# Kernel optimization log

Hardware: AMD Instinct MI355X
Metric: run time of the kernel (lower is better)

The kernel has to match this reference:

```python
import jax, jax.numpy as jnp
import numpy as np

B, T, C = 2, 2048, 1024
N_HEAD = 16
HEAD_DIM = C // N_HEAD


def setup_inputs() -> dict:
    key = jax.random.key(0)
    k1, k2, k3 = jax.random.split(key, 3)
    x = jax.random.normal(k1, (B, T, C), dtype=jnp.float32)
    w_qkv = jax.random.normal(k2, (C, 3 * C), dtype=jnp.float32) * (C ** -0.5)
    w_proj = jax.random.normal(k3, (C, C), dtype=jnp.float32) * (C ** -0.5)
    b_proj = jnp.zeros((C,), dtype=jnp.float32)
    return {"x": x, "w_qkv": w_qkv, "w_proj": w_proj, "b_proj": b_proj}


def reference(x, w_qkv, w_proj, b_proj):
    Bx, Tx, Cx = x.shape
    # qkv projection: [B,T,3C] -> split into q,k,v each [B,H,T,D]
    qkv = x @ w_qkv  # [B,T,3C]
    qkv = qkv.reshape(Bx, Tx, 3, N_HEAD, HEAD_DIM)
    q = qkv[:, :, 0].transpose(0, 2, 1, 3)  # [B,H,T,D]
    k = qkv[:, :, 1].transpose(0, 2, 1, 3)
    v = qkv[:, :, 2].transpose(0, 2, 1, 3)
    scale = 1.0 / np.sqrt(HEAD_DIM).astype(np.float32)
    att = jnp.einsum('bhtd,bhsd->bhts', q, k) * scale  # [B,H,T,T]
    causal = jnp.tril(jnp.ones((Tx, Tx), dtype=bool))
    att = jnp.where(causal[None, None], att, -jnp.inf)
    att = jax.nn.softmax(att, axis=-1)
    # dropout p=0.0 -> identity (eval-mode math)
    y = jnp.einsum('bhts,bhsd->bhtd', att, v)  # [B,H,T,D]
    y = y.transpose(0, 2, 1, 3).reshape(Bx, Tx, Cx)
    return y @ w_proj + b_proj
```

## Files before the change

### kernel.cpp

```cpp
#include <hip/hip_runtime.h>

typedef __bf16 bf16x8 __attribute__((ext_vector_type(8)));
typedef float f32x4 __attribute__((ext_vector_type(4)));
typedef unsigned short u16;
typedef unsigned int u32;
typedef u32 u32x4 __attribute__((ext_vector_type(4)));
typedef u16 u16x8 __attribute__((ext_vector_type(8)));

#define B_ 2
#define T_ 2048
#define C_ 1024
#define H_ 16
#define D_ 64
#define QSCALE 0.18033688011112042f

__device__ __forceinline__ u16 f2bf(float f) {
    u32 u = __builtin_bit_cast(u32, f);
    u += 0x7fffu + ((u >> 16) & 1u);
    return (u16)(u >> 16);
}

__device__ __forceinline__ f32x4 mfma16(bf16x8 a, bf16x8 b, f32x4 c) {
    return __builtin_amdgcn_mfma_f32_16x16x32_bf16(a, b, c, 0, 0, 0);
}

__device__ __forceinline__ void gll16(const u16* g, u16* l) {
    __builtin_amdgcn_global_load_lds((const __attribute__((address_space(1))) unsigned int*)g,
                                     (__attribute__((address_space(3))) unsigned int*)l,
                                     16, 0, 0);
}

__global__ __launch_bounds__(256) void prep_kernel(const float* __restrict__ x,
                                                   const float* __restrict__ w_qkv,
                                                   const float* __restrict__ w_proj,
                                                   u16* __restrict__ x_bf,
                                                   u16* __restrict__ wqkv_t,
                                                   u16* __restrict__ wproj_t) {
    __shared__ float tile[64][65];
    int bid = blockIdx.x;
    int t = threadIdx.x;
    if (bid < 1024) {
        int base = bid * 4096 + t * 4;
#pragma unroll
        for (int it = 0; it < 4; ++it) {
            int i = base + it * 1024;
            float4 v = *(const float4*)(x + i);
            x_bf[i + 0] = f2bf(v.x);
            x_bf[i + 1] = f2bf(v.y);
            x_bf[i + 2] = f2bf(v.z);
            x_bf[i + 3] = f2bf(v.w);
        }
        return;
    }
    const float* in;
    u16* out;
    int N, tidx;
    if (bid < 1792) { in = w_qkv; out = wqkv_t; N = 3 * C_; tidx = bid - 1024; }
    else            { in = w_proj; out = wproj_t; N = C_;  tidx = bid - 1792; }
    int ntiles = N / 64;
    int n0 = (tidx % ntiles) * 64, k0 = (tidx / ntiles) * 64;
    int c = t & 63, r0 = t >> 6;
    for (int i = 0; i < 16; ++i) {
        int r = r0 * 16 + i;
        tile[r][c] = in[(size_t)(k0 + r) * N + n0 + c];
    }
    __syncthreads();
    for (int i = 0; i < 16; ++i) {
        int rn = r0 * 16 + i;
        out[(size_t)(n0 + rn) * C_ + k0 + c] = f2bf(tile[c][rn]);
    }
}

__global__ __launch_bounds__(256) void qkv_gemm(const u16* __restrict__ x_bf,
                                                const u16* __restrict__ wqkv_t,
                                                u16* __restrict__ Qo, u16* __restrict__ Ko,
                                                u16* __restrict__ Vto) {
    __shared__ __align__(16) u16 smem[8192];
    u16* As = smem;
    u16* Bs = smem + 4096;
    const int K = 1024;
    int bid = blockIdx.x;
    bool qk = (bid < 512);
    const u16 *A, *Bt;
    int m0, n0;
    if (qk) {
        A = x_bf; Bt = wqkv_t;
        n0 = (bid & 15) * 128; m0 = (bid >> 4) * 128;
    } else {
        int vb = bid - 512;
        A = wqkv_t + 2048 * 1024; Bt = x_bf;
        n0 = (vb & 31) * 128; m0 = (vb >> 5) * 128;
    }
    int t = threadIdx.x;
    int wave = t >> 6, lane = t & 63, lr = lane & 15, quad = lane >> 4;
    int wm = (wave >> 1) * 64, wn = (wave & 1) * 64;

    int srow = lane >> 2;
    int sgl = (lane & 3) ^ (srow & 3);

    f32x4 acc[4][4];
    for (int i = 0; i < 4; ++i)
        for (int j = 0; j < 4; ++j) acc[i][j] = (f32x4){0.f, 0.f, 0.f, 0.f};

    int swz = (quad ^ (lr & 3)) * 8;

    for (int kb = 0; kb < K; kb += 32) {
        __syncthreads();
        for (int i = 0; i < 2; ++i) {
            int c = wave * 2 + i;
            int row = c * 16 + srow;
            gll16(&A[(size_t)(m0 + row) * K + kb + sgl * 8], &As[c * 512]);
            gll16(&Bt[(size_t)(n0 + row) * K + kb + sgl * 8], &Bs[c * 512]);
        }
        __syncthreads();
        bf16x8 af[4], bfr[4];
        for (int mt = 0; mt < 4; ++mt)
            af[mt] = *(const bf16x8*)&As[(wm + mt * 16 + lr) * 32 + swz];
        for (int nt = 0; nt < 4; ++nt)
            bfr[nt] = *(const bf16x8*)&Bs[(wn + nt * 16 + lr) * 32 + swz];
        for (int mt = 0; mt < 4; ++mt)
            for (int nt = 0; nt < 4; ++nt) acc[mt][nt] = mfma16(af[mt], bfr[nt], acc[mt][nt]);
    }

    __syncthreads();
    u16* eb = smem + wave * 1152;
    int row = lane >> 2;
    int cb = (lane & 3) * 16;
    if (qk) {
        int colg = n0 + wn;
        int part = colg >> 10;
        int h = (colg & 1023) >> 6;
        float sc = (part == 0) ? QSCALE : 1.0f;
        u16* outb = (part == 0) ? Qo : Ko;
#pragma unroll
        for (int p = 0; p < 4; ++p) {
            asm volatile("" ::: "memory");
#pragma unroll
            for (int nt = 0; nt < 4; ++nt)
#pragma unroll
                for (int r = 0; r < 4; ++r)
                    eb[(quad * 4 + r) * 72 + nt * 16 + lr] = f2bf(acc[p][nt][r] * sc);
            asm volatile("" ::: "memory");
            u16x8 va = *(const u16x8*)(eb + row * 72 + cb);
            u16x8 vb = *(const u16x8*)(eb + row * 72 + cb + 8);
            asm volatile("" ::: "memory");
            int rowg = m0 + wm + p * 16 + row;
            int bb = rowg >> 11, tt = rowg & 2047;
            int bh = bb * H_ + h;
            u32* dst = (u32*)(outb + ((size_t)(bh * T_ + tt)) * D_ + cb);
            *(u32x4*)dst = __builtin_bit_cast(u32x4, va);
            *(u32x4*)(dst + 4) = __builtin_bit_cast(u32x4, vb);
        }
    } else {
#pragma unroll
        for (int p = 0; p < 4; ++p) {
            asm volatile("" ::: "memory");
#pragma unroll
            for (int nt = 0; nt < 4; ++nt)
#pragma unroll
                for (int r = 0; r < 4; ++r)
                    eb[(quad * 4 + r) * 72 + nt * 16 + lr] = f2bf(acc[p][nt][r]);
            asm volatile("" ::: "memory");
            u16x8 va = *(const u16x8*)(eb + row * 72 + cb);
            u16x8 vb = *(const u16x8*)(eb + row * 72 + cb + 8);
            asm volatile("" ::: "memory");
            int rowg = m0 + wm + p * 16 + row;
            int h = rowg >> 6, d = rowg & 63;
            int tg = n0 + wn + cb;
            int bb = tg >> 11, tt = tg & 2047;
            u32* dst = (u32*)(Vto + (((size_t)(bb * H_ + h)) * D_ + d) * T_ + tt);
            *(u32x4*)dst = __builtin_bit_cast(u32x4, va);
            *(u32x4*)(dst + 4) = __builtin_bit_cast(u32x4, vb);
        }
    }
}

__global__ __launch_bounds__(256) void gemm64_proj(const u16* __restrict__ A,
                                                   const u16* __restrict__ Bt,
                                                   float* __restrict__ Cout,
                                                   const float* __restrict__ bias,
                                                   int M, int N, int K) {
    __shared__ __align__(16) u16 smem[6144];
    u16* As = smem;
    u16* Bs = smem + 4096;
    int m0 = blockIdx.y * 128, n0 = blockIdx.x * 64;
    int t = threadIdx.x;
    int wave = t >> 6, lane = t & 63, lr = lane & 15, quad = lane >> 4;
    int srow = lane >> 2;
    int sgl = (lane & 3) ^ (srow & 3);
    int swz = (quad ^ (lr & 3)) * 8;

    f32x4 acc[2][4];
#pragma unroll
    for (int i = 0; i < 2; ++i)
#pragma unroll
        for (int j = 0; j < 4; ++j) acc[i][j] = (f32x4){0.f, 0.f, 0.f, 0.f};

    for (int kb = 0; kb < K; kb += 32) {
        __syncthreads();
#pragma unroll
        for (int i = 0; i < 2; ++i) {
            int c = wave * 2 + i;
            int row = c * 16 + srow;
            gll16(&A[(size_t)(m0 + row) * K + kb + sgl * 8], &As[c * 512]);
        }
        {
            int row = wave * 16 + srow;
            gll16(&Bt[(size_t)(n0 + row) * K + kb + sgl * 8], &Bs[wave * 512]);
        }
        __syncthreads();
        bf16x8 af[2], bfr[4];
#pragma unroll
        for (int mt = 0; mt < 2; ++mt)
            af[mt] = *(const bf16x8*)&As[(wave * 32 + mt * 16 + lr) * 32 + swz];
#pragma unroll
        for (int nt = 0; nt < 4; ++nt)
            bfr[nt] = *(const bf16x8*)&Bs[(nt * 16 + lr) * 32 + swz];
#pragma unroll
        for (int mt = 0; mt < 2; ++mt)
#pragma unroll
            for (int nt = 0; nt < 4; ++nt) acc[mt][nt] = mfma16(af[mt], bfr[nt], acc[mt][nt]);
    }

#pragma unroll
    for (int mt = 0; mt < 2; ++mt)
#pragma unroll
        for (int nt = 0; nt < 4; ++nt)
#pragma unroll
            for (int r = 0; r < 4; ++r) {
                int rowg = m0 + wave * 32 + mt * 16 + quad * 4 + r;
                int col = n0 + nt * 16 + lr;
                Cout[(size_t)rowg * N + col] = acc[mt][nt][r] + bias[col];
            }
}

__global__ __launch_bounds__(256, 4) void attn_kernel(const u16* __restrict__ Q,
                                                      const u16* __restrict__ Kb,
                                                      const u16* __restrict__ Vt,
                                                      u16* __restrict__ Y) {
    __shared__ __align__(16) u16 Kls[2][64 * 64];
    __shared__ __align__(16) u16 Vls[2][64 * 64];
    __shared__ __align__(16) u32 Pls[4][512];
    int qt = 31 - (blockIdx.x >> 5);
    int bh = blockIdx.x & 31;
    int t = threadIdx.x, wave = t >> 6, lane = t & 63, lr = lane & 15, quad = lane >> 4;

    const u16* kbase = Kb + (size_t)bh * (T_ * D_);
    const u16* vbase = Vt + (size_t)bh * (D_ * T_);
    const u16* Qg = Q + ((size_t)bh * T_ + qt * 64 + wave * 16 + lr) * D_;
    bf16x8 qfl = *(const bf16x8*)(Qg + quad * 8);
    bf16x8 qfh = *(const bf16x8*)(Qg + 32 + quad * 8);

    float lsum = 0.f;
    f32x4 o[4];
#pragma unroll
    for (int dt = 0; dt < 4; ++dt) o[dt] = (f32x4){0.f, 0.f, 0.f, 0.f};

    int srow = lane >> 3;
    int sgl = (lane & 7) ^ srow;
    int swz1 = (quad ^ (lr & 7)) * 8;
    int swz2 = ((quad + 4) ^ (lr & 7)) * 8;
    u32* pw = &Pls[wave][0];
    int pwbase = lr * 32 + (quad & 1) * 2;
    int rg1 = (quad ^ (lr & 7)) << 2;
    int rg2 = ((quad + 4) ^ (lr & 7)) << 2;

    for (int i = 0; i < 2; ++i) {
        int c = wave * 2 + i;
        int row = c * 8 + srow;
        gll16(kbase + (size_t)row * D_ + sgl * 8, &Kls[0][c * 512]);
        gll16(vbase + (size_t)row * T_ + sgl * 8, &Vls[0][c * 512]);
    }

    for (int kt = 0; kt <= qt; ++kt) {
        int buf = kt & 1;
        __syncthreads();
        if (kt < qt) {
            int nk = kt + 1;
            for (int i = 0; i < 2; ++i) {
                int c = wave * 2 + i;
                int row = c * 8 + srow;
                gll16(kbase + (size_t)(nk * 64 + row) * D_ + sgl * 8, &Kls[buf ^ 1][c * 512]);
                gll16(vbase + (size_t)row * T_ + nk * 64 + sgl * 8, &Vls[buf ^ 1][c * 512]);
            }
        }
        bf16x8 kf0[4], kf1[4], vf0[4], vf1[4];
#pragma unroll
        for (int st = 0; st < 4; ++st) {
            const u16* kp = &Kls[buf][(st * 16 + lr) * 64];
            kf0[st] = *(const bf16x8*)(kp + swz1);
            kf1[st] = *(const bf16x8*)(kp + swz2);
            const u16* vp = &Vls[buf][(st * 16 + lr) * 64];
            vf0[st] = *(const bf16x8*)(vp + swz1);
            vf1[st] = *(const bf16x8*)(vp + swz2);
        }
        f32x4 s[4];
#pragma unroll
        for (int st = 0; st < 4; ++st) {
            s[st] = mfma16(kf0[st], qfl, (f32x4){0.f, 0.f, 0.f, 0.f});
            s[st] = mfma16(kf1[st], qfh, s[st]);
        }
        if (kt == qt) {
            int qloc = wave * 16 + lr;
#pragma unroll
            for (int st = 0; st < 4; ++st)
#pragma unroll
                for (int r = 0; r < 4; ++r) {
                    if (st * 16 + quad * 4 + r > qloc) s[st][r] = -__builtin_inff();
                }
        }
        float sum = 0.f;
#pragma unroll
        for (int st = 0; st < 4; ++st)
#pragma unroll
            for (int r = 0; r < 4; ++r) {
                float p = __builtin_amdgcn_exp2f(s[st][r]);
                s[st][r] = p;
                sum += p;
            }
        sum += __shfl_xor(sum, 16);
        sum += __shfl_xor(sum, 32);
        lsum += sum;
        asm volatile("" ::: "memory");
#pragma unroll
        for (int st = 0; st < 4; ++st)
#pragma unroll
            for (int rp = 0; rp < 2; ++rp) {
                u32 lo = f2bf(s[st][2 * rp]);
                u32 hi = f2bf(s[st][2 * rp + 1]);
                pw[pwbase + (((st * 2 + (quad >> 1)) ^ (lr & 7)) << 2) + rp] = lo | (hi << 16);
            }
        asm volatile("" ::: "memory");
        const u32* prow = &pw[lr * 32];
        u32x4 plo = *(const u32x4*)(prow + rg1);
        u32x4 phi = *(const u32x4*)(prow + rg2);
        asm volatile("" ::: "memory");
        bf16x8 pfl = __builtin_bit_cast(bf16x8, plo);
        bf16x8 pfh = __builtin_bit_cast(bf16x8, phi);
#pragma unroll
        for (int dt = 0; dt < 4; ++dt) {
            o[dt] = mfma16(vf0[dt], pfl, o[dt]);
            o[dt] = mfma16(vf1[dt], pfh, o[dt]);
        }
    }

    int b = bh >> 4, h = bh & 15;
    float inv = 1.0f / lsum;
    asm volatile("" ::: "memory");
#pragma unroll
    for (int dt = 0; dt < 4; ++dt)
#pragma unroll
        for (int rp = 0; rp < 2; ++rp) {
            u32 lo = f2bf(o[dt][2 * rp] * inv);
            u32 hi = f2bf(o[dt][2 * rp + 1] * inv);
            pw[pwbase + (((dt * 2 + (quad >> 1)) ^ (lr & 7)) << 2) + rp] = lo | (hi << 16);
        }
    asm volatile("" ::: "memory");
    {
        int query = lane >> 2, wsel = lane & 3;
        const u32* prow = &pw[query * 32];
        u32x4 w0 = *(const u32x4*)(prow + (((wsel * 2) ^ (query & 7)) << 2));
        u32x4 w1 = *(const u32x4*)(prow + (((wsel * 2 + 1) ^ (query & 7)) << 2));
        u32* dst = (u32*)(Y + ((size_t)(b * T_ + qt * 64 + wave * 16 + query)) * C_ + h * 64 + wsel * 16);
        *(u32x4*)dst = w0;
        *(u32x4*)(dst + 4) = w1;
    }
}

extern "C" void kernel_launch(void* const* d_in, const int* in_sizes, int n_in,
                              void* d_out, int out_size, void* d_ws, size_t ws_size,
                              hipStream_t stream) {
    const float* x      = (const float*)d_in[0];
    const float* w_qkv  = (const float*)d_in[1];
    const float* w_proj = (const float*)d_in[2];
    const float* b_proj = (const float*)d_in[3];
    float* out = (float*)d_out;

    char* ws = (char*)d_ws;
    u16* x_bf    = (u16*)(ws + 0);
    u16* wqkv_t  = (u16*)(ws + 8388608);
    u16* wproj_t = (u16*)(ws + 14680064);
    u16* q_bf    = (u16*)(ws + 16777216);
    u16* k_bf    = (u16*)(ws + 25165824);
    u16* vt_bf   = (u16*)(ws + 33554432);
    u16* y_bf    = (u16*)(ws + 41943040);

    const int M = B_ * T_;

    prep_kernel<<<2048, 256, 0, stream>>>(x, w_qkv, w_proj, x_bf, wqkv_t, wproj_t);

    qkv_gemm<<<768, 256, 0, stream>>>(x_bf, wqkv_t, q_bf, k_bf, vt_bf);

    attn_kernel<<<32 * (T_ / 64), 256, 0, stream>>>(q_bf, k_bf, vt_bf, y_bf);

    gemm64_proj<<<dim3(C_ / 64, M / 128), 256, 0, stream>>>(
        y_bf, wproj_t, out, b_proj, M, C_, C_);
}
```

Before: 184.1 us.

## Double-buffer LDS tiles in QKV and projection GEMMs and change swizzle

Both the QKV and output-projection GEMMs now use two LDS buffers. The next K-slice is loaded asynchronously while MFMAs run on the current one, and each iteration needs one barrier instead of two. The LDS XOR swizzle is also changed to key on row pairs, which is meant to reduce bank conflicts for the 16-row fragment reads. This doubles LDS usage per block, which may lower occupancy.

New measurement: 169.8 us. 1.08x faster.

```diff
diff --git a/kernel.cpp b/kernel.cpp
--- a/kernel.cpp
+++ b/kernel.cpp
@@ -75,9 +75,7 @@
                                                 const u16* __restrict__ wqkv_t,
                                                 u16* __restrict__ Qo, u16* __restrict__ Ko,
                                                 u16* __restrict__ Vto) {
-    __shared__ __align__(16) u16 smem[8192];
-    u16* As = smem;
-    u16* Bs = smem + 4096;
+    __shared__ __align__(16) u16 smem[16384];
     const int K = 1024;
     int bid = blockIdx.x;
     bool qk = (bid < 512);
@@ -96,23 +94,31 @@
     int wm = (wave >> 1) * 64, wn = (wave & 1) * 64;
 
     int srow = lane >> 2;
-    int sgl = (lane & 3) ^ (srow & 3);
+    int sgl = (lane & 3) ^ ((srow >> 1) & 3);
+    int swz = (quad ^ ((lr >> 1) & 3)) * 8;
 
     f32x4 acc[4][4];
     for (int i = 0; i < 4; ++i)
         for (int j = 0; j < 4; ++j) acc[i][j] = (f32x4){0.f, 0.f, 0.f, 0.f};
 
-    int swz = (quad ^ (lr & 3)) * 8;
-
-    for (int kb = 0; kb < K; kb += 32) {
-        __syncthreads();
+    auto stage = [&](int b, int kb) {
+        u16* As = smem + b * 4096;
+        u16* Bs = smem + 8192 + b * 4096;
         for (int i = 0; i < 2; ++i) {
             int c = wave * 2 + i;
             int row = c * 16 + srow;
             gll16(&A[(size_t)(m0 + row) * K + kb + sgl * 8], &As[c * 512]);
             gll16(&Bt[(size_t)(n0 + row) * K + kb + sgl * 8], &Bs[c * 512]);
         }
+    };
+
+    stage(0, 0);
+    for (int kt = 0; kt < 32; ++kt) {
+        int buf = kt & 1;
         __syncthreads();
+        if (kt < 31) stage(buf ^ 1, (kt + 1) * 32);
+        const u16* As = smem + buf * 4096;
+        const u16* Bs = smem + 8192 + buf * 4096;
         bf16x8 af[4], bfr[4];
         for (int mt = 0; mt < 4; ++mt)
             af[mt] = *(const bf16x8*)&As[(wm + mt * 16 + lr) * 32 + swz];
@@ -180,15 +186,13 @@
                                                    float* __restrict__ Cout,
                                                    const float* __restrict__ bias,
                                                    int M, int N, int K) {
-    __shared__ __align__(16) u16 smem[6144];
-    u16* As = smem;
-    u16* Bs = smem + 4096;
+    __shared__ __align__(16) u16 smem[12288];
     int m0 = blockIdx.y * 128, n0 = blockIdx.x * 64;
     int t = threadIdx.x;
     int wave = t >> 6, lane = t & 63, lr = lane & 15, quad = lane >> 4;
     int srow = lane >> 2;
-    int sgl = (lane & 3) ^ (srow & 3);
-    int swz = (quad ^ (lr & 3)) * 8;
+    int sgl = (lane & 3) ^ ((srow >> 1) & 3);
+    int swz = (quad ^ ((lr >> 1) & 3)) * 8;
 
     f32x4 acc[2][4];
 #pragma unroll
@@ -196,8 +200,9 @@
 #pragma unroll
         for (int j = 0; j < 4; ++j) acc[i][j] = (f32x4){0.f, 0.f, 0.f, 0.f};
 
-    for (int kb = 0; kb < K; kb += 32) {
-        __syncthreads();
+    auto stage = [&](int b, int kb) {
+        u16* As = smem + b * 4096;
+        u16* Bs = smem + 8192 + b * 2048;
 #pragma unroll
         for (int i = 0; i < 2; ++i) {
             int c = wave * 2 + i;
@@ -208,7 +213,16 @@
             int row = wave * 16 + srow;
             gll16(&Bt[(size_t)(n0 + row) * K + kb + sgl * 8], &Bs[wave * 512]);
         }
+    };
+
+    int niter = K / 32;
+    stage(0, 0);
+    for (int kt = 0; kt < niter; ++kt) {
+        int buf = kt & 1;
         __syncthreads();
+        if (kt < niter - 1) stage(buf ^ 1, (kt + 1) * 32);
+        const u16* As = smem + buf * 4096;
+        const u16* Bs = smem + 8192 + buf * 2048;
         bf16x8 af[2], bfr[4];
 #pragma unroll
         for (int mt = 0; mt < 2; ++mt)
```
